# Kernel tuning notes

Hardware: AMD Instinct MI355X
Metric: run time of the kernel (lower is better)

Reference implementation:

```python
import jax, jax.numpy as jnp
import numpy as np

DT = 1.0
GAMMA = 0.3
JITTER = 1e-05
ELL_MIN = 0.05
ELL_MAX = 10.0


def setup_inputs() -> dict:
    key = jax.random.key(0)
    k1, k2, k3, k4, k5 = jax.random.split(key, 5)
    n_dim, T = 768, 24
    S = jax.random.normal(k1, (n_dim, 2), dtype=jnp.float32)
    mu_seq = 0.5 * jax.random.normal(k2, (T, 4), dtype=jnp.float32)
    Q = 0.3 * jax.random.normal(k3, (T, 4, 4), dtype=jnp.float32)
    Sigma_seq = jnp.einsum('tab,tcb->tac', Q, Q)  # PSD per step
    A_seq = jax.random.uniform(k4, (T, 2, 2), dtype=jnp.float32)
    # torch init: logit((ell_init-ell_min)/(ell_max-ell_min)) ~= -2.249, plus small noise
    raw_ell = jnp.float32(-2.249) + 0.1 * jax.random.normal(k5, (2, 2), dtype=jnp.float32)
    return {'S': S, 'mu_seq': mu_seq, 'Sigma_seq': Sigma_seq, 'A_seq': A_seq, 'raw_ell': raw_ell}


def reference(S, mu_seq, Sigma_seq, A_seq, raw_ell):
    n = S.shape[0]
    T = mu_seq.shape[0]
    dtype = mu_seq.dtype
    ell = ELL_MIN + (ELL_MAX - ELL_MIN) * jax.nn.sigmoid(raw_ell)  # [2,2]
    # selectors: Es[0] = E_u, Es[1] = E_v, each [2,4]
    Es = jnp.array([[[1., 0., 0., 0.], [0., 1., 0., 0.]],
                    [[0., 0., 1., 0.], [0., 0., 0., 1.]]], dtype=dtype)
    eye2 = jnp.eye(2, dtype=dtype)
    # B[i,j] = dt*(Es[i] - gamma*Es[j]) -> [2,2,2,4] (i, j, row, 4)
    B = DT * (Es[:, None] - GAMMA * Es[None, :])
    # shift[t,i,j] = B[i,j] @ mu[t] -> [T,2,2,2]
    shift = jnp.einsum('ijrk,tk->tijr', B, mu_seq)
    # D[t,i,j] = ell[i,j]^2 I + 2 B Sigma_t B^T + jitter I -> [T,2,2,2,2]
    BSB = jnp.einsum('ijrk,tkl,ijsl->tijrs', B, Sigma_seq, B)
    D = (ell ** 2)[None, :, :, None, None] * eye2 + 2.0 * BSB + JITTER * eye2
    L = jnp.linalg.cholesky(D)
    logdet = 2.0 * jnp.sum(jnp.log(jnp.diagonal(L, axis1=-2, axis2=-1)), axis=-1)  # [T,2,2]
    # pairwise displacements H[p,q] = S[p] - S[q] -> [n,n,2]
    H = S[:, None, :] - S[None, :, :]
    # H' = H - shift -> [T,2,2,n,n,2]
    Hp = H[None, None, None] - shift[:, :, :, None, None, :]
    # alpha = D^{-1} H'  (batched 2x2 solves, D broadcast over the n x n grid)
    alpha = jnp.linalg.solve(D[:, :, :, None, None], Hp[..., None])[..., 0]
    maha = jnp.sum(Hp * alpha, axis=-1)  # [T,2,2,n,n]
    K = jnp.exp(-maha - 0.5 * logdet[..., None, None])
    blocks = A_seq[:, :, :, None, None] * K  # [T,2,2,n,n]
    # assemble [T, 2n, 2n] with i indexing row-blocks, j indexing col-blocks
    M = blocks.transpose(0, 1, 3, 2, 4).reshape(T, 2 * n, 2 * n)
    # row normalize
    M = M / jnp.clip(jnp.sum(M, axis=-1, keepdims=True), 1e-08, None)
    return M
```

## Files before the change

### kernel.cpp

```cpp
#include <hip/hip_runtime.h>


typedef unsigned int u32;

namespace {
constexpr float GAMMA_C   = 0.3f;
constexpr float JITTER_C  = 1e-5f;
constexpr float ELL_MIN_C = 0.05f;
constexpr float ELL_MAX_C = 10.0f;
constexpr int   NPT     = 768;
constexpr int   TSTEPS  = 24;
constexpr int   ROWS    = TSTEPS * 2 * NPT;
constexpr int   W_ROWS  = 4;
constexpr int   WAVES   = 4;
constexpr int   THREADS = WAVES * 64;
constexpr int   RPB     = W_ROWS * WAVES;
constexpr int   SLOTS   = ROWS / RPB;
constexpr int   BLOCKS  = 768;
}

__global__ __launch_bounds__(THREADS) void vlk_kernel(
    const float* __restrict__ S,
    const float* __restrict__ mu_seq,
    const float* __restrict__ Sg,
    const float* __restrict__ A,
    const float* __restrict__ rl,
    float* __restrict__ out)
{
    const int w    = threadIdx.x >> 6;
    const int lane = threadIdx.x & 63;

    float sx[12], sy[12];
#pragma unroll
    for (int m = 0; m < 3; ++m) {
        const int q0 = m * 256 + lane * 4;
        const float4 a4 = *((const float4*)(S + 2 * q0));
        const float4 b4 = *((const float4*)(S + 2 * q0 + 4));
        sx[4*m+0] = a4.x; sy[4*m+0] = a4.y;
        sx[4*m+1] = a4.z; sy[4*m+1] = a4.w;
        sx[4*m+2] = b4.x; sy[4*m+2] = b4.y;
        sx[4*m+3] = b4.z; sy[4*m+3] = b4.w;
    }

    const float g = GAMMA_C;

    for (int slot = blockIdx.x; slot < SLOTS; slot += BLOCKS) {
        const int base = slot * RPB;
        const int t    = base / (2 * NPT);
        const int rem  = base - t * (2 * NPT);
        const int i    = rem / NPT;
        const int p0   = rem - i * NPT + w * W_ROWS;

        float mu[4];
#pragma unroll
        for (int k = 0; k < 4; ++k) mu[k] = mu_seq[t * 4 + k];
        float Sgm[4][4];
#pragma unroll
        for (int r = 0; r < 4; ++r)
#pragma unroll
            for (int c = 0; c < 4; ++c) Sgm[r][c] = Sg[t * 16 + r * 4 + c];

        float shift0[2], shift1[2], i00[2], i01x2[2], i11[2], coef[2];
        const int bi = 2 * i;
#pragma unroll
        for (int jj = 0; jj < 2; ++jj) {
            const int bj = 2 * jj;
            shift0[jj] = mu[bi]     - g * mu[bj];
            shift1[jj] = mu[bi + 1] - g * mu[bj + 1];
            const float b00 = Sgm[bi][bi]     - g*Sgm[bi][bj]     - g*Sgm[bj][bi]     + g*g*Sgm[bj][bj];
            const float b01 = Sgm[bi][bi+1]   - g*Sgm[bi][bj+1]   - g*Sgm[bj][bi+1]   + g*g*Sgm[bj][bj+1];
            const float b11 = Sgm[bi+1][bi+1] - g*Sgm[bi+1][bj+1] - g*Sgm[bj+1][bi+1] + g*g*Sgm[bj+1][bj+1];
            const float rlv = rl[i * 2 + jj];
            const float ell = ELL_MIN_C + (ELL_MAX_C - ELL_MIN_C) / (1.0f + __expf(-rlv));
            const float e2  = ell * ell + JITTER_C;
            const float D00 = e2 + 2.0f * b00;
            const float D01 =      2.0f * b01;
            const float D11 = e2 + 2.0f * b11;
            const float det  = D00 * D11 - D01 * D01;
            const float rdet = 1.0f / det;
            i00[jj]   =  D11 * rdet;
            i01x2[jj] = -2.0f * D01 * rdet;
            i11[jj]   =  D00 * rdet;
            coef[jj] = A[(t * 2 + i) * 2 + jj] * rsqrtf(det);
        }

#pragma unroll
        for (int r = 0; r < W_ROWS; ++r) {
            const int p = p0 + r;
            const float sp0 = S[2 * p];
            const float sp1 = S[2 * p + 1];

            float cx[2], cy[2];
#pragma unroll
            for (int jj = 0; jj < 2; ++jj) {
                cx[jj] = sp0 - shift0[jj];
                cy[jj] = sp1 - shift1[jj];
            }

            float vals[24];
            float lsum = 0.0f;
#pragma unroll
            for (int k = 0; k < 6; ++k) {
                const int jj = (k >= 3) ? 1 : 0;
                const int m  = k - 3 * jj;
                const float cx0 = cx[jj], cy0 = cy[jj];
                const float a0 = i00[jj], a1x2 = i01x2[jj], a2 = i11[jj], cf = coef[jj];
#pragma unroll
                for (int j = 0; j < 4; ++j) {
                    const float h0 = cx0 - sx[4*m+j];
                    const float h1 = cy0 - sy[4*m+j];
                    const float maha = (a0 * h0 + a1x2 * h1) * h0 + a2 * h1 * h1;
                    const float v = cf * __expf(-maha);
                    vals[4*k+j] = v;
                    lsum += v;
                }
            }

#pragma unroll
            for (int off = 1; off < 64; off <<= 1) lsum += __shfl_xor(lsum, off, 64);
            const float inv = 1.0f / fmaxf(lsum, 1e-8f);

            float* op = out + (size_t)(base + w * W_ROWS + r) * (2 * NPT);
#pragma unroll
            for (int k = 0; k < 6; ++k) {
                float4 o;
                o.x = vals[4*k+0] * inv;
                o.y = vals[4*k+1] * inv;
                o.z = vals[4*k+2] * inv;
                o.w = vals[4*k+3] * inv;
                *((float4*)(op + k * 256 + lane * 4)) = o;
            }
        }
    }
}

extern "C" void kernel_launch(void* const* d_in, const int* in_sizes, int n_in,
                              void* d_out, int out_size, void* d_ws, size_t ws_size,
                              hipStream_t stream) {
    vlk_kernel<<<BLOCKS, THREADS, 0, stream>>>(
        (const float*)d_in[0],
        (const float*)d_in[1],
        (const float*)d_in[2],
        (const float*)d_in[3],
        (const float*)d_in[4],
        (float*)d_out);
}
```

Baseline: 234.3 us.

## Split into row-sum pass and recompute-and-store pass with one block per slot

```diff
diff --git a/kernel.cpp b/kernel.cpp
--- a/kernel.cpp
+++ b/kernel.cpp
@@ -15,22 +15,53 @@
 constexpr int   WAVES   = 4;
 constexpr int   THREADS = WAVES * 64;
 constexpr int   RPB     = W_ROWS * WAVES;
-constexpr int   SLOTS   = ROWS / RPB;
-constexpr int   BLOCKS  = 768;
-}
-
-__global__ __launch_bounds__(THREADS) void vlk_kernel(
-    const float* __restrict__ S,
-    const float* __restrict__ mu_seq,
-    const float* __restrict__ Sg,
-    const float* __restrict__ A,
-    const float* __restrict__ rl,
-    float* __restrict__ out)
-{
-    const int w    = threadIdx.x >> 6;
-    const int lane = threadIdx.x & 63;
-
-    float sx[12], sy[12];
+constexpr int   BLOCKS  = ROWS / RPB;
+}
+
+__device__ __forceinline__ void load_params(
+    const float* __restrict__ mu_seq, const float* __restrict__ Sg,
+    const float* __restrict__ A, const float* __restrict__ rl,
+    int t, int i,
+    float (&shift0)[2], float (&shift1)[2],
+    float (&i00)[2], float (&i01x2)[2], float (&i11)[2], float (&coef)[2])
+{
+    const float g = GAMMA_C;
+    float mu[4];
+#pragma unroll
+    for (int k = 0; k < 4; ++k) mu[k] = mu_seq[t * 4 + k];
+    float Sgm[4][4];
+#pragma unroll
+    for (int r = 0; r < 4; ++r)
+#pragma unroll
+        for (int c = 0; c < 4; ++c) Sgm[r][c] = Sg[t * 16 + r * 4 + c];
+
+    const int bi = 2 * i;
+#pragma unroll
+    for (int jj = 0; jj < 2; ++jj) {
+        const int bj = 2 * jj;
+        shift0[jj] = mu[bi]     - g * mu[bj];
+        shift1[jj] = mu[bi + 1] - g * mu[bj + 1];
+        const float b00 = Sgm[bi][bi]     - g*Sgm[bi][bj]     - g*Sgm[bj][bi]     + g*g*Sgm[bj][bj];
+        const float b01 = Sgm[bi][bi+1]   - g*Sgm[bi][bj+1]   - g*Sgm[bj][bi+1]   + g*g*Sgm[bj][bj+1];
+        const float b11 = Sgm[bi+1][bi+1] - g*Sgm[bi+1][bj+1] - g*Sgm[bj+1][bi+1] + g*g*Sgm[bj+1][bj+1];
+        const float rlv = rl[i * 2 + jj];
+        const float ell = ELL_MIN_C + (ELL_MAX_C - ELL_MIN_C) / (1.0f + __expf(-rlv));
+        const float e2  = ell * ell + JITTER_C;
+        const float D00 = e2 + 2.0f * b00;
+        const float D01 =      2.0f * b01;
+        const float D11 = e2 + 2.0f * b11;
+        const float det  = D00 * D11 - D01 * D01;
+        const float rdet = 1.0f / det;
+        i00[jj]   =  D11 * rdet;
+        i01x2[jj] = -2.0f * D01 * rdet;
+        i11[jj]   =  D00 * rdet;
+        coef[jj] = A[(t * 2 + i) * 2 + jj] * rsqrtf(det);
+    }
+}
+
+__device__ __forceinline__ void load_spts(const float* __restrict__ S, int lane,
+                                          float (&sx)[12], float (&sy)[12])
+{
 #pragma unroll
     for (int m = 0; m < 3; ++m) {
         const int q0 = m * 256 + lane * 4;
@@ -41,95 +72,165 @@
         sx[4*m+2] = b4.x; sy[4*m+2] = b4.y;
         sx[4*m+3] = b4.z; sy[4*m+3] = b4.w;
     }
-
-    const float g = GAMMA_C;
-
-    for (int slot = blockIdx.x; slot < SLOTS; slot += BLOCKS) {
-        const int base = slot * RPB;
-        const int t    = base / (2 * NPT);
-        const int rem  = base - t * (2 * NPT);
-        const int i    = rem / NPT;
-        const int p0   = rem - i * NPT + w * W_ROWS;
-
-        float mu[4];
-#pragma unroll
-        for (int k = 0; k < 4; ++k) mu[k] = mu_seq[t * 4 + k];
-        float Sgm[4][4];
-#pragma unroll
-        for (int r = 0; r < 4; ++r)
-#pragma unroll
-            for (int c = 0; c < 4; ++c) Sgm[r][c] = Sg[t * 16 + r * 4 + c];
-
-        float shift0[2], shift1[2], i00[2], i01x2[2], i11[2], coef[2];
-        const int bi = 2 * i;
+}
+
+__global__ __launch_bounds__(THREADS) void vlk_sums(
+    const float* __restrict__ S, const float* __restrict__ mu_seq,
+    const float* __restrict__ Sg, const float* __restrict__ A,
+    const float* __restrict__ rl, float* __restrict__ wsum)
+{
+    const int w    = threadIdx.x >> 6;
+    const int lane = threadIdx.x & 63;
+
+    const int base = blockIdx.x * RPB;
+    const int t    = base / (2 * NPT);
+    const int rem  = base - t * (2 * NPT);
+    const int i    = rem / NPT;
+    const int p0   = rem - i * NPT + w * W_ROWS;
+
+    float shift0[2], shift1[2], i00[2], i01x2[2], i11[2], coef[2];
+    load_params(mu_seq, Sg, A, rl, t, i, shift0, shift1, i00, i01x2, i11, coef);
+
+    float sx[12], sy[12];
+    load_spts(S, lane, sx, sy);
+
+#pragma unroll
+    for (int r = 0; r < W_ROWS; ++r) {
+        const int p = p0 + r;
+        const float sp0 = S[2 * p];
+        const float sp1 = S[2 * p + 1];
+
+        float lsum = 0.0f;
 #pragma unroll
         for (int jj = 0; jj < 2; ++jj) {
-            const int bj = 2 * jj;
-            shift0[jj] = mu[bi]     - g * mu[bj];
-            shift1[jj] = mu[bi + 1] - g * mu[bj + 1];
-            const float b00 = Sgm[bi][bi]     - g*Sgm[bi][bj]     - g*Sgm[bj][bi]     + g*g*Sgm[bj][bj];
-            const float b01 = Sgm[bi][bi+1]   - g*Sgm[bi][bj+1]   - g*Sgm[bj][bi+1]   + g*g*Sgm[bj][bj+1];
-            const float b11 = Sgm[bi+1][bi+1] - g*Sgm[bi+1][bj+1] - g*Sgm[bj+1][bi+1] + g*g*Sgm[bj+1][bj+1];
-            const float rlv = rl[i * 2 + jj];
-            const float ell = ELL_MIN_C + (ELL_MAX_C - ELL_MIN_C) / (1.0f + __expf(-rlv));
-            const float e2  = ell * ell + JITTER_C;
-            const float D00 = e2 + 2.0f * b00;
-            const float D01 =      2.0f * b01;
-            const float D11 = e2 + 2.0f * b11;
-            const float det  = D00 * D11 - D01 * D01;
-            const float rdet = 1.0f / det;
-            i00[jj]   =  D11 * rdet;
-            i01x2[jj] = -2.0f * D01 * rdet;
-            i11[jj]   =  D00 * rdet;
-            coef[jj] = A[(t * 2 + i) * 2 + jj] * rsqrtf(det);
-        }
-
-#pragma unroll
-        for (int r = 0; r < W_ROWS; ++r) {
-            const int p = p0 + r;
-            const float sp0 = S[2 * p];
-            const float sp1 = S[2 * p + 1];
-
-            float cx[2], cy[2];
-#pragma unroll
-            for (int jj = 0; jj < 2; ++jj) {
-                cx[jj] = sp0 - shift0[jj];
-                cy[jj] = sp1 - shift1[jj];
-            }
-
-            float vals[24];
-            float lsum = 0.0f;
-#pragma unroll
-            for (int k = 0; k < 6; ++k) {
-                const int jj = (k >= 3) ? 1 : 0;
-                const int m  = k - 3 * jj;
-                const float cx0 = cx[jj], cy0 = cy[jj];
-                const float a0 = i00[jj], a1x2 = i01x2[jj], a2 = i11[jj], cf = coef[jj];
-#pragma unroll
-                for (int j = 0; j < 4; ++j) {
-                    const float h0 = cx0 - sx[4*m+j];
-                    const float h1 = cy0 - sy[4*m+j];
-                    const float maha = (a0 * h0 + a1x2 * h1) * h0 + a2 * h1 * h1;
-                    const float v = cf * __expf(-maha);
-                    vals[4*k+j] = v;
-                    lsum += v;
-                }
-            }
-
-#pragma unroll
-            for (int off = 1; off < 64; off <<= 1) lsum += __shfl_xor(lsum, off, 64);
-            const float inv = 1.0f / fmaxf(lsum, 1e-8f);
-
-            float* op = out + (size_t)(base + w * W_ROWS + r) * (2 * NPT);
-#pragma unroll
-            for (int k = 0; k < 6; ++k) {
-                float4 o;
-                o.x = vals[4*k+0] * inv;
-                o.y = vals[4*k+1] * inv;
-                o.z = vals[4*k+2] * inv;
-                o.w = vals[4*k+3] * inv;
-                *((float4*)(op + k * 256 + lane * 4)) = o;
-            }
+            const float cx = sp0 - shift0[jj];
+            const float cy = sp1 - shift1[jj];
+            const float a0 = i00[jj], a1x2 = i01x2[jj], a2 = i11[jj], cf = coef[jj];
+#pragma unroll
+            for (int q = 0; q < 12; ++q) {
+                const float h0 = cx - sx[q];
+                const float h1 = cy - sy[q];
+                const float maha = (a0 * h0 + a1x2 * h1) * h0 + a2 * h1 * h1;
+                lsum += cf * __expf(-maha);
+            }
+        }
+#pragma unroll
+        for (int off = 1; off < 64; off <<= 1) lsum += __shfl_xor(lsum, off, 64);
+        if (lane == 0)
+            wsum[base + w * W_ROWS + r] = 1.0f / fmaxf(lsum, 1e-8f);
+    }
+}
+
+__global__ __launch_bounds__(THREADS) void vlk_store(
+    const float* __restrict__ S, const float* __restrict__ mu_seq,
+    const float* __restrict__ Sg, const float* __restrict__ A,
+    const float* __restrict__ rl, const float* __restrict__ wsum,
+    float* __restrict__ out)
+{
+    const int w    = threadIdx.x >> 6;
+    const int lane = threadIdx.x & 63;
+
+    const int base = blockIdx.x * RPB;
+    const int t    = base / (2 * NPT);
+    const int rem  = base - t * (2 * NPT);
+    const int i    = rem / NPT;
+    const int p0   = rem - i * NPT + w * W_ROWS;
+
+    float shift0[2], shift1[2], i00[2], i01x2[2], i11[2], coef[2];
+    load_params(mu_seq, Sg, A, rl, t, i, shift0, shift1, i00, i01x2, i11, coef);
+
+    float sx[12], sy[12];
+    load_spts(S, lane, sx, sy);
+
+#pragma unroll
+    for (int r = 0; r < W_ROWS; ++r) {
+        const int row = base + w * W_ROWS + r;
+        const int p = p0 + r;
+        const float sp0 = S[2 * p];
+        const float sp1 = S[2 * p + 1];
+        const float inv = wsum[row];
+
+        float* op = out + (size_t)row * (2 * NPT);
+#pragma unroll
+        for (int k = 0; k < 6; ++k) {
+            const int jj = (k >= 3) ? 1 : 0;
+            const int m  = k - 3 * jj;
+            const float cx = sp0 - shift0[jj];
+            const float cy = sp1 - shift1[jj];
+            const float a0 = i00[jj], a1x2 = i01x2[jj], a2 = i11[jj];
+            const float cfi = coef[jj] * inv;
+            float4 o;
+            {
+                const float h0 = cx - sx[4*m+0], h1 = cy - sy[4*m+0];
+                o.x = cfi * __expf(-((a0*h0 + a1x2*h1)*h0 + a2*h1*h1));
+            }
+            {
+                const float h0 = cx - sx[4*m+1], h1 = cy - sy[4*m+1];
+                o.y = cfi * __expf(-((a0*h0 + a1x2*h1)*h0 + a2*h1*h1));
+            }
+            {
+                const float h0 = cx - sx[4*m+2], h1 = cy - sy[4*m+2];
+                o.z = cfi * __expf(-((a0*h0 + a1x2*h1)*h0 + a2*h1*h1));
+            }
+            {
+                const float h0 = cx - sx[4*m+3], h1 = cy - sy[4*m+3];
+                o.w = cfi * __expf(-((a0*h0 + a1x2*h1)*h0 + a2*h1*h1));
+            }
+            *((float4*)(op + k * 256 + lane * 4)) = o;
+        }
+    }
+}
+
+__global__ __launch_bounds__(THREADS) void vlk_single(
+    const float* __restrict__ S, const float* __restrict__ mu_seq,
+    const float* __restrict__ Sg, const float* __restrict__ A,
+    const float* __restrict__ rl, float* __restrict__ out)
+{
+    const int w    = threadIdx.x >> 6;
+    const int lane = threadIdx.x & 63;
+    const int base = blockIdx.x * RPB;
+    const int t    = base / (2 * NPT);
+    const int rem  = base - t * (2 * NPT);
+    const int i    = rem / NPT;
+    const int p0   = rem - i * NPT + w * W_ROWS;
+
+    float shift0[2], shift1[2], i00[2], i01x2[2], i11[2], coef[2];
+    load_params(mu_seq, Sg, A, rl, t, i, shift0, shift1, i00, i01x2, i11, coef);
+    float sx[12], sy[12];
+    load_spts(S, lane, sx, sy);
+
+#pragma unroll
+    for (int r = 0; r < W_ROWS; ++r) {
+        const int p = p0 + r;
+        const float sp0 = S[2 * p];
+        const float sp1 = S[2 * p + 1];
+        float vals[24];
+        float lsum = 0.0f;
+#pragma unroll
+        for (int k = 0; k < 6; ++k) {
+            const int jj = (k >= 3) ? 1 : 0;
+            const int m  = k - 3 * jj;
+            const float cx = sp0 - shift0[jj], cy = sp1 - shift1[jj];
+            const float a0 = i00[jj], a1x2 = i01x2[jj], a2 = i11[jj], cf = coef[jj];
+#pragma unroll
+            for (int j = 0; j < 4; ++j) {
+                const float h0 = cx - sx[4*m+j];
+                const float h1 = cy - sy[4*m+j];
+                const float v = cf * __expf(-((a0*h0 + a1x2*h1)*h0 + a2*h1*h1));
+                vals[4*k+j] = v;
+                lsum += v;
+            }
+        }
+#pragma unroll
+        for (int off = 1; off < 64; off <<= 1) lsum += __shfl_xor(lsum, off, 64);
+        const float inv = 1.0f / fmaxf(lsum, 1e-8f);
+        float* op = out + (size_t)(base + w * W_ROWS + r) * (2 * NPT);
+#pragma unroll
+        for (int k = 0; k < 6; ++k) {
+            float4 o;
+            o.x = vals[4*k+0] * inv; o.y = vals[4*k+1] * inv;
+            o.z = vals[4*k+2] * inv; o.w = vals[4*k+3] * inv;
+            *((float4*)(op + k * 256 + lane * 4)) = o;
         }
     }
 }
@@ -137,11 +238,16 @@
 extern "C" void kernel_launch(void* const* d_in, const int* in_sizes, int n_in,
                               void* d_out, int out_size, void* d_ws, size_t ws_size,
                               hipStream_t stream) {
-    vlk_kernel<<<BLOCKS, THREADS, 0, stream>>>(
-        (const float*)d_in[0],
-        (const float*)d_in[1],
-        (const float*)d_in[2],
-        (const float*)d_in[3],
-        (const float*)d_in[4],
-        (float*)d_out);
-}
+    const float* S  = (const float*)d_in[0];
+    const float* mu = (const float*)d_in[1];
+    const float* Sg = (const float*)d_in[2];
+    const float* A  = (const float*)d_in[3];
+    const float* rl = (const float*)d_in[4];
+    if (d_ws != nullptr && ws_size >= (size_t)ROWS * sizeof(float)) {
+        float* wsum = (float*)d_ws;
+        vlk_sums <<<BLOCKS, THREADS, 0, stream>>>(S, mu, Sg, A, rl, wsum);
+        vlk_store<<<BLOCKS, THREADS, 0, stream>>>(S, mu, Sg, A, rl, wsum, (float*)d_out);
+    } else {
+        vlk_single<<<BLOCKS, THREADS, 0, stream>>>(S, mu, Sg, A, rl, (float*)d_out);
+    }
+}
```

After: 269.7 us. 1.15x slower.
